# Optimization experiments

Hardware: AMD Instinct MI355X
Metric: run time of the kernel (lower is better)

## Reference

```python
import jax, jax.numpy as jnp
import numpy as np

D_MODEL = 768
BOTTLENECK = 64
LN_EPS = 1e-5
SCALE = 1.0


def setup_inputs() -> dict:
    key = jax.random.key(0)
    k_x, k_wd = jax.random.split(key, 2)
    x = jax.random.normal(k_x, (8, 4096, D_MODEL), dtype=jnp.float32)
    # LayerNorm affine params
    ln_gamma = jnp.ones((D_MODEL,), dtype=jnp.float32)
    ln_beta = jnp.zeros((D_MODEL,), dtype=jnp.float32)
    # down_proj: kaiming_uniform_(a=sqrt(5)) -> bound = 1/sqrt(fan_in)
    bound = 1.0 / np.sqrt(D_MODEL)
    w_down = jax.random.uniform(k_wd, (D_MODEL, BOTTLENECK), dtype=jnp.float32,
                                minval=-bound, maxval=bound)
    b_down = jnp.zeros((BOTTLENECK,), dtype=jnp.float32)
    # up_proj initialized to zeros per 'lora' init; use small nonzero to make grads informative?
    # Stay faithful: zeros, as in the module's init.
    w_up = jnp.zeros((BOTTLENECK, D_MODEL), dtype=jnp.float32)
    b_up = jnp.zeros((D_MODEL,), dtype=jnp.float32)
    return {"x": x, "ln_gamma": ln_gamma, "ln_beta": ln_beta,
            "w_down": w_down, "b_down": b_down, "w_up": w_up, "b_up": b_up}


def _layer_norm(x, gamma, beta):
    mean = jnp.mean(x, axis=-1, keepdims=True)
    var = jnp.var(x, axis=-1, keepdims=True)
    return (x - mean) * jax.lax.rsqrt(var + LN_EPS) * gamma + beta


def reference(x, ln_gamma, ln_beta, w_down, b_down, w_up, b_up):
    # adapter_layernorm_option == 'in': LN before down projection
    h = _layer_norm(x, ln_gamma, ln_beta)              # [B, S, D]
    down = jnp.einsum('bsd,dk->bsk', h, w_down) + b_down  # [B, S, K]
    down = jax.nn.relu(down)
    # dropout is identity in eval mode
    out = jnp.einsum('bsk,kd->bsd', down, w_up) + b_up    # [B, S, D]
    return out * SCALE
```

## Files before the change

### kernel.cpp

```cpp
#include <hip/hip_runtime.h>
#include <hip/hip_bf16.h>


#define D_MODEL 768
#define KB      64
#define BM      16
#define NTHR    256

typedef __attribute__((ext_vector_type(8))) short    bf16x8;
typedef __attribute__((ext_vector_type(4))) float    f32x4;
typedef __attribute__((ext_vector_type(4))) unsigned short us4;

static __device__ __forceinline__ unsigned short f2bf(float f) {
  unsigned int u = __builtin_bit_cast(unsigned int, f);
  unsigned int r = u + 0x7FFFu + ((u >> 16) & 1u);
  return (unsigned short)(r >> 16);
}

__global__ void adapter_prep(const float* __restrict__ wd,
                             const float* __restrict__ wu,
                             const float* __restrict__ gamma,
                             const float* __restrict__ beta,
                             const float* __restrict__ bdown,
                             unsigned short* __restrict__ wdT,
                             unsigned short* __restrict__ wuT,
                             float* __restrict__ s_arr,
                             float* __restrict__ t_arr) {
  const int b = blockIdx.x;
  const int t = threadIdx.x;
  if (b < 192) {
    const int i = b * 256 + t;
    const int k1 = i / D_MODEL;
    const int d1 = i - k1 * D_MODEL;
    wdT[i] = f2bf(gamma[d1] * wd[(size_t)d1 * KB + k1]);
    const int d2 = i >> 6;
    const int k2 = i & 63;
    wuT[i] = f2bf(wu[(size_t)k2 * D_MODEL + d2]);
  } else {
    const int k = t & 63;
    const int c = t >> 6;
    float ss = 0.f, tt = 0.f;
    const int d0 = c * 192;
    #pragma unroll 4
    for (int d = d0; d < d0 + 192; ++d) {
      const float w = wd[(size_t)d * KB + k];
      ss = fmaf(gamma[d], w, ss);
      tt = fmaf(beta[d],  w, tt);
    }
    __shared__ float ps[4][64], pt[4][64];
    ps[c][k] = ss; pt[c][k] = tt;
    __syncthreads();
    if (t < 64) {
      s_arr[t] = ps[0][t] + ps[1][t] + ps[2][t] + ps[3][t];
      t_arr[t] = pt[0][t] + pt[1][t] + pt[2][t] + pt[3][t] + bdown[t];
    }
  }
}

#define XPAD 776
#define PPAD 72

__global__ void __launch_bounds__(NTHR, 6) adapter_main(
    const float* __restrict__ x,
    const float* __restrict__ s_arr,
    const float* __restrict__ t_arr,
    const unsigned short* __restrict__ wdT,
    const unsigned short* __restrict__ wuT,
    const float* __restrict__ b_up,
    float* __restrict__ out) {

  __shared__ unsigned short x_s[BM * XPAD];
  __shared__ unsigned short p_s[BM * PPAD];
  __shared__ float mu_s[BM];
  __shared__ float rs_s[BM];

  const int t    = threadIdx.x;
  const int row0 = blockIdx.x * BM;

  {
    const int r  = t >> 4;
    const int c0 = (t & 15) * 4;
    const float* xp = x + (size_t)(row0 + r) * D_MODEL;
    float s1 = 0.f, s2 = 0.f;
    #pragma unroll
    for (int i = 0; i < 12; ++i) {
      const int c = c0 + 64 * i;
      const float4 v = *(const float4*)(xp + c);
      s1 += v.x + v.y + v.z + v.w;
      s2 = fmaf(v.x, v.x, s2); s2 = fmaf(v.y, v.y, s2);
      s2 = fmaf(v.z, v.z, s2); s2 = fmaf(v.w, v.w, s2);
      us4 pk;
      pk.x = f2bf(v.x); pk.y = f2bf(v.y); pk.z = f2bf(v.z); pk.w = f2bf(v.w);
      *(us4*)&x_s[r * XPAD + c] = pk;
    }
    s1 += __shfl_xor(s1, 1); s2 += __shfl_xor(s2, 1);
    s1 += __shfl_xor(s1, 2); s2 += __shfl_xor(s2, 2);
    s1 += __shfl_xor(s1, 4); s2 += __shfl_xor(s2, 4);
    s1 += __shfl_xor(s1, 8); s2 += __shfl_xor(s2, 8);
    const float mean = s1 * (1.0f / 768.0f);
    const float var  = s2 * (1.0f / 768.0f) - mean * mean;
    if ((t & 15) == 0) {
      mu_s[r] = mean;
      rs_s[r] = rsqrtf(var + 1e-5f);
    }
  }
  __syncthreads();

  const int w  = t >> 6;
  const int l  = t & 63;
  const int lr = l & 15;
  const int lg = l >> 4;

  {
    const int cw = 16 * w;
    f32x4 acc = {0.f, 0.f, 0.f, 0.f};
    const unsigned short* bp = wdT + (size_t)(cw + lr) * D_MODEL + 8 * lg;
    #pragma unroll
    for (int kk = 0; kk < 24; ++kk) {
      const bf16x8 bq = *(const bf16x8*)(bp + 32 * kk);
      const bf16x8 a0 = *(const bf16x8*)&x_s[lr * XPAD + 32 * kk + 8 * lg];
      acc = __builtin_amdgcn_mfma_f32_16x16x32_bf16(a0, bq, acc, 0, 0, 0);
    }
    const float sk = s_arr[cw + lr];
    const float tk = t_arr[cw + lr];
    #pragma unroll
    for (int j = 0; j < 4; ++j) {
      const int r = 4 * lg + j;
      const float rs = rs_s[r], mu = mu_s[r];
      float dn = fmaf(rs, acc[j], fmaf(-rs * mu, sk, tk));
      dn = fmaxf(dn, 0.0f);
      p_s[r * PPAD + cw + lr] = f2bf(dn);
    }
  }
  __syncthreads();

  {
    const bf16x8 pa0 = *(const bf16x8*)&p_s[lr * PPAD + 8 * lg];
    const bf16x8 pa1 = *(const bf16x8*)&p_s[lr * PPAD + 32 + 8 * lg];
    #pragma unroll
    for (int i = 0; i < 12; ++i) {
      const int cn = 16 * (12 * w + i);
      const unsigned short* bp2 = wuT + (size_t)(cn + lr) * KB + 8 * lg;
      const bf16x8 b0 = *(const bf16x8*)(bp2);
      const bf16x8 b1 = *(const bf16x8*)(bp2 + 32);
      f32x4 c0 = {0.f, 0.f, 0.f, 0.f};
      c0 = __builtin_amdgcn_mfma_f32_16x16x32_bf16(pa0, b0, c0, 0, 0, 0);
      c0 = __builtin_amdgcn_mfma_f32_16x16x32_bf16(pa1, b1, c0, 0, 0, 0);
      const float bu = b_up[cn + lr];
      #pragma unroll
      for (int j = 0; j < 4; ++j) {
        out[(size_t)(row0 + 4 * lg + j) * D_MODEL + cn + lr] = c0[j] + bu;
      }
    }
  }
}

extern "C" void kernel_launch(void* const* d_in, const int* in_sizes, int n_in,
                              void* d_out, int out_size, void* d_ws, size_t ws_size,
                              hipStream_t stream) {
  const float* x     = (const float*)d_in[0];
  const float* gamma = (const float*)d_in[1];
  const float* beta  = (const float*)d_in[2];
  const float* wd    = (const float*)d_in[3];
  const float* bdown = (const float*)d_in[4];
  const float* wu    = (const float*)d_in[5];
  const float* bup   = (const float*)d_in[6];
  float* out = (float*)d_out;

  char* ws = (char*)d_ws;
  unsigned short* wdT = (unsigned short*)ws;
  unsigned short* wuT = (unsigned short*)(ws + 98304);
  float* s_arr = (float*)(ws + 196608);
  float* t_arr = (float*)(ws + 196864);

  const int rows = in_sizes[0] / D_MODEL;

  adapter_prep<<<193, NTHR, 0, stream>>>(wd, wu, gamma, beta, bdown,
                                         wdT, wuT, s_arr, t_arr);
  adapter_main<<<rows / BM, NTHR, 0, stream>>>(x, s_arr, t_arr, wdT, wuT, bup, out);
}
```

Measured before the change: 241.4 us.

## Give each wave its own 16-row tile and feed x straight from registers

The block now covers 64 rows, with each wave owning 16 rows. Each wave loads x from global memory directly into MFMA operand registers and computes the LayerNorm statistics along the way. The x staging buffer in shared memory and one barrier are gone, and each wave computes all 64 bottleneck columns with four accumulators. The trade-off is heavier per-wave register use (launch bounds drop to 4) and x loads of only 32 bytes per lane per step rather than coalesced float4 sweeps.

```diff
diff --git a/kernel.cpp b/kernel.cpp
--- a/kernel.cpp
+++ b/kernel.cpp
@@ -4,8 +4,8 @@
 
 #define D_MODEL 768
 #define KB      64
-#define BM      16
 #define NTHR    256
+#define PPAD    72
 
 typedef __attribute__((ext_vector_type(8))) short    bf16x8;
 typedef __attribute__((ext_vector_type(4))) float    f32x4;
@@ -57,10 +57,7 @@
   }
 }
 
-#define XPAD 776
-#define PPAD 72
-
-__global__ void __launch_bounds__(NTHR, 6) adapter_main(
+__global__ void __launch_bounds__(NTHR, 4) adapter_main(
     const float* __restrict__ x,
     const float* __restrict__ s_arr,
     const float* __restrict__ t_arr,
@@ -69,89 +66,84 @@
     const float* __restrict__ b_up,
     float* __restrict__ out) {
 
-  __shared__ unsigned short x_s[BM * XPAD];
-  __shared__ unsigned short p_s[BM * PPAD];
-  __shared__ float mu_s[BM];
-  __shared__ float rs_s[BM];
+  __shared__ unsigned short p_s[4][16][PPAD];
 
-  const int t    = threadIdx.x;
-  const int row0 = blockIdx.x * BM;
+  const int t   = threadIdx.x;
+  const int wid = t >> 6;
+  const int l   = t & 63;
+  const int lr  = l & 15;
+  const int lg  = l >> 4;
+  const int row0 = blockIdx.x * 64 + wid * 16;
 
-  {
-    const int r  = t >> 4;
-    const int c0 = (t & 15) * 4;
-    const float* xp = x + (size_t)(row0 + r) * D_MODEL;
-    float s1 = 0.f, s2 = 0.f;
-    #pragma unroll
-    for (int i = 0; i < 12; ++i) {
-      const int c = c0 + 64 * i;
-      const float4 v = *(const float4*)(xp + c);
-      s1 += v.x + v.y + v.z + v.w;
-      s2 = fmaf(v.x, v.x, s2); s2 = fmaf(v.y, v.y, s2);
-      s2 = fmaf(v.z, v.z, s2); s2 = fmaf(v.w, v.w, s2);
-      us4 pk;
-      pk.x = f2bf(v.x); pk.y = f2bf(v.y); pk.z = f2bf(v.z); pk.w = f2bf(v.w);
-      *(us4*)&x_s[r * XPAD + c] = pk;
-    }
-    s1 += __shfl_xor(s1, 1); s2 += __shfl_xor(s2, 1);
-    s1 += __shfl_xor(s1, 2); s2 += __shfl_xor(s2, 2);
-    s1 += __shfl_xor(s1, 4); s2 += __shfl_xor(s2, 4);
-    s1 += __shfl_xor(s1, 8); s2 += __shfl_xor(s2, 8);
-    const float mean = s1 * (1.0f / 768.0f);
-    const float var  = s2 * (1.0f / 768.0f) - mean * mean;
-    if ((t & 15) == 0) {
-      mu_s[r] = mean;
-      rs_s[r] = rsqrtf(var + 1e-5f);
-    }
+  const float* xp = x + (size_t)(row0 + lr) * D_MODEL + 8 * lg;
+  const unsigned short* wp = wdT + (size_t)lr * D_MODEL + 8 * lg;
+
+  f32x4 acc0 = {0.f,0.f,0.f,0.f}, acc1 = {0.f,0.f,0.f,0.f};
+  f32x4 acc2 = {0.f,0.f,0.f,0.f}, acc3 = {0.f,0.f,0.f,0.f};
+  float s1 = 0.f, s2 = 0.f;
+
+  #pragma unroll
+  for (int kk = 0; kk < 24; ++kk) {
+    const float4 v0 = *(const float4*)(xp + 32 * kk);
+    const float4 v1 = *(const float4*)(xp + 32 * kk + 4);
+    s1 += (v0.x + v0.y) + (v0.z + v0.w) + (v1.x + v1.y) + (v1.z + v1.w);
+    s2 = fmaf(v0.x, v0.x, s2); s2 = fmaf(v0.y, v0.y, s2);
+    s2 = fmaf(v0.z, v0.z, s2); s2 = fmaf(v0.w, v0.w, s2);
+    s2 = fmaf(v1.x, v1.x, s2); s2 = fmaf(v1.y, v1.y, s2);
+    s2 = fmaf(v1.z, v1.z, s2); s2 = fmaf(v1.w, v1.w, s2);
+    bf16x8 xf;
+    xf[0] = (short)f2bf(v0.x); xf[1] = (short)f2bf(v0.y);
+    xf[2] = (short)f2bf(v0.z); xf[3] = (short)f2bf(v0.w);
+    xf[4] = (short)f2bf(v1.x); xf[5] = (short)f2bf(v1.y);
+    xf[6] = (short)f2bf(v1.z); xf[7] = (short)f2bf(v1.w);
+    const bf16x8 wa0 = *(const bf16x8*)(wp + 32 * kk);
+    const bf16x8 wa1 = *(const bf16x8*)(wp + 16 * D_MODEL + 32 * kk);
+    const bf16x8 wa2 = *(const bf16x8*)(wp + 32 * D_MODEL + 32 * kk);
+    const bf16x8 wa3 = *(const bf16x8*)(wp + 48 * D_MODEL + 32 * kk);
+    acc0 = __builtin_amdgcn_mfma_f32_16x16x32_bf16(wa0, xf, acc0, 0, 0, 0);
+    acc1 = __builtin_amdgcn_mfma_f32_16x16x32_bf16(wa1, xf, acc1, 0, 0, 0);
+    acc2 = __builtin_amdgcn_mfma_f32_16x16x32_bf16(wa2, xf, acc2, 0, 0, 0);
+    acc3 = __builtin_amdgcn_mfma_f32_16x16x32_bf16(wa3, xf, acc3, 0, 0, 0);
   }
+
+  s1 += __shfl_xor(s1, 16); s1 += __shfl_xor(s1, 32);
+  s2 += __shfl_xor(s2, 16); s2 += __shfl_xor(s2, 32);
+  const float mu  = s1 * (1.0f / 768.0f);
+  const float var = s2 * (1.0f / 768.0f) - mu * mu;
+  const float rs  = rsqrtf(var + 1e-5f);
+  const float nm  = -rs * mu;
+
+  #pragma unroll
+  for (int c = 0; c < 4; ++c) {
+    const f32x4 a = (c == 0) ? acc0 : (c == 1) ? acc1 : (c == 2) ? acc2 : acc3;
+    const float4 sv = *(const float4*)(s_arr + 16 * c + 4 * lg);
+    const float4 tv = *(const float4*)(t_arr + 16 * c + 4 * lg);
+    us4 pk;
+    pk.x = f2bf(fmaxf(fmaf(rs, a[0], fmaf(nm, sv.x, tv.x)), 0.f));
+    pk.y = f2bf(fmaxf(fmaf(rs, a[1], fmaf(nm, sv.y, tv.y)), 0.f));
+    pk.z = f2bf(fmaxf(fmaf(rs, a[2], fmaf(nm, sv.z, tv.z)), 0.f));
+    pk.w = f2bf(fmaxf(fmaf(rs, a[3], fmaf(nm, sv.w, tv.w)), 0.f));
+    *(us4*)&p_s[wid][lr][16 * c + 4 * lg] = pk;
+  }
+
   __syncthreads();
 
-  const int w  = t >> 6;
-  const int l  = t & 63;
-  const int lr = l & 15;
-  const int lg = l >> 4;
+  const bf16x8 pa0 = *(const bf16x8*)&p_s[wid][lr][8 * lg];
+  const bf16x8 pa1 = *(const bf16x8*)&p_s[wid][lr][32 + 8 * lg];
+  float* op = out + (size_t)(row0 + 4 * lg) * D_MODEL + lr;
 
-  {
-    const int cw = 16 * w;
-    f32x4 acc = {0.f, 0.f, 0.f, 0.f};
-    const unsigned short* bp = wdT + (size_t)(cw + lr) * D_MODEL + 8 * lg;
-    #pragma unroll
-    for (int kk = 0; kk < 24; ++kk) {
-      const bf16x8 bq = *(const bf16x8*)(bp + 32 * kk);
-      const bf16x8 a0 = *(const bf16x8*)&x_s[lr * XPAD + 32 * kk + 8 * lg];
-      acc = __builtin_amdgcn_mfma_f32_16x16x32_bf16(a0, bq, acc, 0, 0, 0);
-    }
-    const float sk = s_arr[cw + lr];
-    const float tk = t_arr[cw + lr];
-    #pragma unroll
-    for (int j = 0; j < 4; ++j) {
-      const int r = 4 * lg + j;
-      const float rs = rs_s[r], mu = mu_s[r];
-      float dn = fmaf(rs, acc[j], fmaf(-rs * mu, sk, tk));
-      dn = fmaxf(dn, 0.0f);
-      p_s[r * PPAD + cw + lr] = f2bf(dn);
-    }
-  }
-  __syncthreads();
-
-  {
-    const bf16x8 pa0 = *(const bf16x8*)&p_s[lr * PPAD + 8 * lg];
-    const bf16x8 pa1 = *(const bf16x8*)&p_s[lr * PPAD + 32 + 8 * lg];
-    #pragma unroll
-    for (int i = 0; i < 12; ++i) {
-      const int cn = 16 * (12 * w + i);
-      const unsigned short* bp2 = wuT + (size_t)(cn + lr) * KB + 8 * lg;
-      const bf16x8 b0 = *(const bf16x8*)(bp2);
-      const bf16x8 b1 = *(const bf16x8*)(bp2 + 32);
-      f32x4 c0 = {0.f, 0.f, 0.f, 0.f};
-      c0 = __builtin_amdgcn_mfma_f32_16x16x32_bf16(pa0, b0, c0, 0, 0, 0);
-      c0 = __builtin_amdgcn_mfma_f32_16x16x32_bf16(pa1, b1, c0, 0, 0, 0);
-      const float bu = b_up[cn + lr];
-      #pragma unroll
-      for (int j = 0; j < 4; ++j) {
-        out[(size_t)(row0 + 4 * lg + j) * D_MODEL + cn + lr] = c0[j] + bu;
-      }
-    }
+  #pragma unroll 4
+  for (int n = 0; n < 48; ++n) {
+    const int cn = 16 * n;
+    const unsigned short* bp = wuT + (size_t)(cn + lr) * KB + 8 * lg;
+    f32x4 c0 = {0.f, 0.f, 0.f, 0.f};
+    c0 = __builtin_amdgcn_mfma_f32_16x16x32_bf16(pa0, *(const bf16x8*)(bp), c0, 0, 0, 0);
+    c0 = __builtin_amdgcn_mfma_f32_16x16x32_bf16(pa1, *(const bf16x8*)(bp + 32), c0, 0, 0, 0);
+    const float bu = b_up[cn + lr];
+    op[(size_t)0 * D_MODEL + cn] = c0[0] + bu;
+    op[(size_t)1 * D_MODEL + cn] = c0[1] + bu;
+    op[(size_t)2 * D_MODEL + cn] = c0[2] + bu;
+    op[(size_t)3 * D_MODEL + cn] = c0[3] + bu;
   }
 }
 
@@ -177,5 +169,5 @@
 
   adapter_prep<<<193, NTHR, 0, stream>>>(wd, wu, gamma, beta, bdown,
                                          wdT, wuT, s_arr, t_arr);
-  adapter_main<<<rows / BM, NTHR, 0, stream>>>(x, s_arr, t_arr, wdT, wuT, bup, out);
+  adapter_main<<<rows / 64, NTHR, 0, stream>>>(x, s_arr, t_arr, wdT, wuT, bup, out);
 }
```

New measurement: 224.5 us. 7.0% less time.
